# Kernel optimization log

Measured on AMD Instinct MI355X. Metric: run time of the kernel, lower is better.

Reference implementation:

```python
import jax, jax.numpy as jnp
import numpy as np

N_ENC = 500_000
N_PAT = 100_000
D_IN = 64
HID = 128
E = 1_000_000


def _seg_mean(x_src, src, dst, n_dst):
    # gather source features along edges, then segment-mean onto destinations
    msg = x_src[src]                                          # [E, d]
    s = jax.ops.segment_sum(msg, dst, num_segments=n_dst)     # [n_dst, d]
    cnt = jax.ops.segment_sum(jnp.ones((src.shape[0], 1), x_src.dtype), dst,
                              num_segments=n_dst)             # [n_dst, 1]
    return s / jnp.maximum(cnt, 1.0)


def _sage(x_src, x_dst, src, dst, n_dst, Wl, Wr, b):
    # PyG SAGEConv: lin_l(mean_aggr(x_j)) + lin_r(x_i); lin_l has bias, lin_r none
    agg = _seg_mean(x_src, src, dst, n_dst)
    return agg @ Wl + b + x_dst @ Wr


def setup_inputs() -> dict:
    key = jax.random.key(0)
    ks = jax.random.split(key, 24)
    sc = 0.05
    inp = {
        "x_enc": jax.random.normal(ks[0], (N_ENC, D_IN), jnp.float32),
        "x_pat": jax.random.normal(ks[1], (N_PAT, D_IN), jnp.float32),
        "src_pe": jax.random.randint(ks[2], (E,), 0, N_PAT),
        "dst_pe": jax.random.randint(ks[3], (E,), 0, N_ENC),
        "src_ep": jax.random.randint(ks[4], (E,), 0, N_ENC),
        "dst_ep": jax.random.randint(ks[5], (E,), 0, N_PAT),
        # layer 1, per edge type
        "Wl_pe1": jax.random.normal(ks[6], (D_IN, HID), jnp.float32) * sc,
        "Wr_pe1": jax.random.normal(ks[7], (D_IN, HID), jnp.float32) * sc,
        "b_pe1": jnp.zeros((HID,), jnp.float32),
        "Wl_ep1": jax.random.normal(ks[8], (D_IN, HID), jnp.float32) * sc,
        "Wr_ep1": jax.random.normal(ks[9], (D_IN, HID), jnp.float32) * sc,
        "b_ep1": jnp.zeros((HID,), jnp.float32),
        # layer 2, per edge type
        "Wl_pe2": jax.random.normal(ks[10], (HID, HID), jnp.float32) * sc,
        "Wr_pe2": jax.random.normal(ks[11], (HID, HID), jnp.float32) * sc,
        "b_pe2": jnp.zeros((HID,), jnp.float32),
        "Wl_ep2": jax.random.normal(ks[12], (HID, HID), jnp.float32) * sc,
        "Wr_ep2": jax.random.normal(ks[13], (HID, HID), jnp.float32) * sc,
        "b_ep2": jnp.zeros((HID,), jnp.float32),
        # classifier
        "Wc": jax.random.normal(ks[14], (HID, 1), jnp.float32) * sc,
        "bc": jnp.zeros((1,), jnp.float32),
    }
    return inp


def reference(x_enc, x_pat, src_pe, dst_pe, src_ep, dst_ep,
              Wl_pe1, Wr_pe1, b_pe1, Wl_ep1, Wr_ep1, b_ep1,
              Wl_pe2, Wr_pe2, b_pe2, Wl_ep2, Wr_ep2, b_ep2,
              Wc, bc):
    # layer 1 (hetero: one SAGEConv per edge type; each node type has one incoming relation)
    h_enc = jax.nn.relu(_sage(x_pat, x_enc, src_pe, dst_pe, N_ENC, Wl_pe1, Wr_pe1, b_pe1))
    h_pat = jax.nn.relu(_sage(x_enc, x_pat, src_ep, dst_ep, N_PAT, Wl_ep1, Wr_ep1, b_ep1))
    # layer 2
    h_enc2 = _sage(h_pat, h_enc, src_pe, dst_pe, N_ENC, Wl_pe2, Wr_pe2, b_pe2)
    # classifier on encounter nodes -> flat logits
    logit = (h_enc2 @ Wc + bc).reshape(-1)                    # [N_ENC]
    return logit
```

## Files before the change

### kernel.cpp

```cpp
#include <hip/hip_runtime.h>
#include <hip/hip_bf16.h>

#define N_ENC 500000
#define N_PAT 100000
#define N_TOT 600000
#define D 64
#define HID 128
#define NE 1000000

#define NB_ENC 245
#define NB 441
#define CAP 8192
#define CH 8192

typedef unsigned short ushort_t;
typedef unsigned int uint_t;
typedef __attribute__((ext_vector_type(8))) short bfrag8;
typedef __attribute__((ext_vector_type(4))) float f32x4;

#define OFF_CURSOR   0
#define ZERO_FLOATS  512
#define OFF_BBASE    512
#define OFF_BASE     1024
#define OFF_CSR      601056
#define OFF_XBF_ENC  2601056
#define OFF_BIN      2601056
#define OFF_XBF_PAT  18601056
#define OFF_SPAT     21801056
#define OFF_FRAGS    21901056
#define OFF_WL2C     21917440
#define OFF_WR2C     21917568
#define OFF_C0       21917696

__device__ inline ushort_t f2bf(float x) {
    uint_t u = __float_as_uint(x);
    u += 0x7fffu + ((u >> 16) & 1u);
    return (ushort_t)(u >> 16);
}

__global__ __launch_bounds__(256) void prep_kernel(
    const float* __restrict__ Wl_pe1, const float* __restrict__ Wr_pe1,
    const float* __restrict__ Wl_ep1, const float* __restrict__ Wr_ep1,
    const float* __restrict__ Wl_pe2, const float* __restrict__ Wr_pe2,
    const float* __restrict__ b_pe2, const float* __restrict__ Wc,
    const float* __restrict__ bc, float* __restrict__ ws)
{
    int t = blockIdx.x * blockDim.x + threadIdx.x;
    const int total = 4 * 8192;
    ushort_t* fr = (ushort_t*)(ws + OFF_FRAGS);
    for (int i = t; i < total; i += gridDim.x * blockDim.x) {
        int mtx = i >> 13;
        int r = i & 8191;
        int jj = r & 7;
        int l = (r >> 3) & 63;
        int ft = r >> 9;
        int kt = ft & 1;
        int jt = ft >> 1;
        int k = kt * 32 + (l >> 4) * 8 + jj;
        int j = jt * 16 + (l & 15);
        const float* W = (mtx == 0) ? Wl_pe1 : (mtx == 1) ? Wr_pe1
                       : (mtx == 2) ? Wl_ep1 : Wr_ep1;
        fr[i] = f2bf(W[k * HID + j]);
    }
    if (blockIdx.x == 0) {
        int tid = threadIdx.x;
        if (tid < HID) {
            float s1 = 0.f, s2 = 0.f;
            for (int j = 0; j < HID; j++) {
                float wc = Wc[j];
                s1 += Wl_pe2[tid * HID + j] * wc;
                s2 += Wr_pe2[tid * HID + j] * wc;
            }
            ws[OFF_WL2C + tid] = s1;
            ws[OFF_WR2C + tid] = s2;
            if (tid == 0) {
                float c0 = bc[0];
                for (int j = 0; j < HID; j++) c0 += b_pe2[j] * Wc[j];
                ws[OFF_C0] = c0;
            }
        }
    }
}

__global__ __launch_bounds__(256) void cvt_bf16_all_kernel(
    const float* __restrict__ x_enc, const float* __restrict__ x_pat,
    ushort_t* __restrict__ xbf_enc, ushort_t* __restrict__ xbf_pat)
{
    const int n8_enc = N_ENC * D / 8;
    const int n8_tot = n8_enc + N_PAT * D / 8;
    int stride = gridDim.x * 256;
    for (int i = blockIdx.x * 256 + threadIdx.x; i < n8_tot; i += stride) {
        const float* in; ushort_t* outp; int j;
        if (i < n8_enc) { in = x_enc; outp = xbf_enc; j = i; }
        else            { in = x_pat; outp = xbf_pat; j = i - n8_enc; }
        const f32x4* p = (const f32x4*)(in + (size_t)j * 8);
        f32x4 v0 = p[0], v1 = p[1];
        uint4 o;
        o.x = (uint_t)f2bf(v0[0]) | ((uint_t)f2bf(v0[1]) << 16);
        o.y = (uint_t)f2bf(v0[2]) | ((uint_t)f2bf(v0[3]) << 16);
        o.z = (uint_t)f2bf(v1[0]) | ((uint_t)f2bf(v1[1]) << 16);
        o.w = (uint_t)f2bf(v1[2]) | ((uint_t)f2bf(v1[3]) << 16);
        *(uint4*)(outp + (size_t)j * 8) = o;
    }
}


__global__ __launch_bounds__(256) void bin_kernel(
    const int* __restrict__ src_pe, const int* __restrict__ dst_pe,
    const int* __restrict__ src_ep, const int* __restrict__ dst_ep,
    int* __restrict__ cursor, uint_t* __restrict__ bin)
{
    __shared__ int lhist[512];
    __shared__ int lbase[512];
    __shared__ int lcnt2[NB];
    __shared__ int gpos[NB];
    __shared__ int s[256];
    __shared__ uint_t lout[CH];
    int t = threadIdx.x;
    int e0 = blockIdx.x * CH;
    int n = min(CH, 2 * NE - e0);

    for (int i = t; i < 512; i += 256) lhist[i] = 0;
    for (int i = t; i < NB; i += 256) lcnt2[i] = 0;
    __syncthreads();
    for (int i = t; i < n; i += 256) {
        int e = e0 + i;
        int dc = (e < NE) ? dst_pe[e] : N_ENC + dst_ep[e - NE];
        int b = (dc < N_ENC) ? (dc >> 11) : (NB_ENC + ((dc - N_ENC) >> 9));
        atomicAdd(&lhist[b], 1);
    }
    __syncthreads();
    int a0 = lhist[2 * t], a1 = lhist[2 * t + 1];
    s[t] = a0 + a1;
    __syncthreads();
    for (int off = 1; off < 256; off <<= 1) {
        int u = (t >= off) ? s[t - off] : 0;
        __syncthreads();
        s[t] += u;
        __syncthreads();
    }
    int ex = s[t] - a0 - a1;
    lbase[2 * t] = ex;
    lbase[2 * t + 1] = ex + a0;
    __syncthreads();
    for (int b = t; b < NB; b += 256) {
        int c = lhist[b];
        if (c) gpos[b] = atomicAdd(&cursor[b], c);
    }
    __syncthreads();
    for (int i = t; i < n; i += 256) {
        int e = e0 + i;
        int dc, sv;
        if (e < NE) { dc = dst_pe[e]; sv = src_pe[e]; }
        else { dc = N_ENC + dst_ep[e - NE]; sv = src_ep[e - NE]; }
        int b, loc;
        if (dc < N_ENC) { b = dc >> 11; loc = dc & 2047; }
        else { b = NB_ENC + ((dc - N_ENC) >> 9); loc = (dc - N_ENC) & 511; }
        int r = atomicAdd(&lcnt2[b], 1);
        lout[lbase[b] + r] = (uint_t)sv | ((uint_t)loc << 20);
    }
    __syncthreads();
    int wv = t >> 6, ln = t & 63;
    for (int b = wv; b < NB; b += 4) {
        int c = lhist[b];
        if (!c) continue;
        int gp = gpos[b];
        int c2 = min(c, CAP - gp);
        if (c2 <= 0) continue;
        uint_t* dstp = bin + (size_t)b * CAP + gp;
        const uint_t* srcp = lout + lbase[b];
        for (int k = ln; k < c2; k += 64) dstp[k] = srcp[k];
    }
}

__global__ __launch_bounds__(256) void bucketscan_kernel(
    const int* __restrict__ cursor, int* __restrict__ bbase,
    int* __restrict__ base)
{
    __shared__ int s[256];
    __shared__ int c2[512];
    int t = threadIdx.x;
    for (int i = t; i < 512; i += 256) c2[i] = (i < NB) ? min(cursor[i], CAP) : 0;
    __syncthreads();
    int a0 = c2[2 * t], a1 = c2[2 * t + 1];
    s[t] = a0 + a1;
    __syncthreads();
    for (int off = 1; off < 256; off <<= 1) {
        int u = (t >= off) ? s[t - off] : 0;
        __syncthreads();
        s[t] += u;
        __syncthreads();
    }
    int ex = s[t] - a0 - a1;
    if (2 * t < NB) bbase[2 * t] = ex;
    if (2 * t + 1 < NB) bbase[2 * t + 1] = ex + a0;
    if (t == 255) { bbase[NB] = s[t]; base[N_TOT] = s[t]; }
}

__global__ __launch_bounds__(256) void csrbuild_kernel(
    const uint_t* __restrict__ bin, const int* __restrict__ cursor,
    const int* __restrict__ bbase, int* __restrict__ base,
    int* __restrict__ csr)
{
    __shared__ int h[2048];
    __shared__ int nb_[2048];
    __shared__ int s[256];
    __shared__ uint_t lout[CAP];
    int b = blockIdx.x;
    int t = threadIdx.x;
    int cnt = min(cursor[b], CAP);
    int nodes_base, nnodes;
    if (b < NB_ENC) { nodes_base = b << 11; nnodes = min(2048, N_ENC - nodes_base); }
    else { nodes_base = N_ENC + ((b - NB_ENC) << 9); nnodes = min(512, N_TOT - nodes_base); }
    const uint_t* reg = bin + (size_t)b * CAP;

    for (int i = t; i < 2048; i += 256) h[i] = 0;
    __syncthreads();
    for (int i = t; i < cnt; i += 256) atomicAdd(&h[reg[i] >> 20], 1);
    __syncthreads();
    int loc[8];
    int sum = 0;
#pragma unroll
    for (int j = 0; j < 8; j++) { loc[j] = sum; sum += h[8 * t + j]; }
    s[t] = sum;
    __syncthreads();
    for (int off = 1; off < 256; off <<= 1) {
        int u = (t >= off) ? s[t - off] : 0;
        __syncthreads();
        s[t] += u;
        __syncthreads();
    }
    int ex = s[t] - sum;
#pragma unroll
    for (int j = 0; j < 8; j++) nb_[8 * t + j] = ex + loc[j];
    __syncthreads();
    int gb = bbase[b];
    for (int i = t; i < nnodes; i += 256) base[nodes_base + i] = gb + nb_[i];
    for (int i = t; i < 2048; i += 256) h[i] = 0;
    __syncthreads();
    for (int i = t; i < cnt; i += 256) {
        uint_t p = reg[i];
        int lc = p >> 20;
        int r = atomicAdd(&h[lc], 1);
        lout[nb_[lc] + r] = p & 0xFFFFFu;
    }
    __syncthreads();
    for (int k = t; k < cnt; k += 256) csr[gb + k] = (int)lout[k];
}

__global__ __launch_bounds__(256) void transform_fused_kernel(
    const ushort_t* __restrict__ xsrc, const int* __restrict__ csr,
    const int* __restrict__ base, const ushort_t* __restrict__ xdst,
    const ushort_t* __restrict__ fragWl, const ushort_t* __restrict__ fragWr,
    const float* __restrict__ bias, const float* __restrict__ cvec,
    const float* __restrict__ sval, const float* __restrict__ c0p,
    float* __restrict__ out, int nwaves, int add_extra)
{
    int wid = blockIdx.x * 4 + (threadIdx.x >> 6);
    if (wid >= nwaves) return;
    int l = threadIdx.x & 63;
    int m = l & 15;
    int q = l >> 4;
    int nb = wid * 16;
    int row = nb + m;

    int s0 = base[row], s1 = base[row + 1];
    float degf = (float)(s1 - s0);

    const ushort_t* xd = xdst + (size_t)row * D;
    bfrag8 x0 = *(const bfrag8*)(xd + q * 8);
    bfrag8 x1 = *(const bfrag8*)(xd + 32 + q * 8);

    float accf[16];
#pragma unroll
    for (int i = 0; i < 16; i++) accf[i] = 0.f;
    float sa = 0.f;

    int s1m1 = s1 - 1;
    for (int e = s0; e < s1; e += 4) {
        int sidx[4];
#pragma unroll
        for (int i = 0; i < 4; i++) {
            int ee = e + i;
            sidx[i] = csr[ee < s1m1 ? ee : s1m1];
        }
        uint4 w0[4], w1[4];
        float sv[4];
#pragma unroll
        for (int i = 0; i < 4; i++) {
            const uint_t* xr = (const uint_t*)(xsrc + (size_t)sidx[i] * D);
            w0[i] = *(const uint4*)(xr + q * 4);
            w1[i] = *(const uint4*)(xr + 16 + q * 4);
            sv[i] = (add_extra && q == 0) ? sval[sidx[i]] : 0.f;
        }
#pragma unroll
        for (int i = 0; i < 4; i++) {
            if (e + i < s1) {
                uint_t dw[8] = {w0[i].x, w0[i].y, w0[i].z, w0[i].w,
                                w1[i].x, w1[i].y, w1[i].z, w1[i].w};
#pragma unroll
                for (int k = 0; k < 8; k++) {
                    accf[2 * k]     += __uint_as_float(dw[k] << 16);
                    accf[2 * k + 1] += __uint_as_float(dw[k] & 0xffff0000u);
                }
                sa += sv[i];
            }
        }
    }

    bfrag8 a0, a1;
#pragma unroll
    for (int i = 0; i < 8; i++) {
        a0[i] = (short)f2bf(accf[i]);
        a1[i] = (short)f2bf(accf[8 + i]);
    }

    float bias_v[8], cvec_v[8];
#pragma unroll
    for (int jt = 0; jt < 8; jt++) {
        bias_v[jt] = bias[jt * 16 + m];
        cvec_v[jt] = cvec[jt * 16 + m];
    }

    f32x4 invc4;
#pragma unroll
    for (int r = 0; r < 4; r++) {
        float dg = __shfl(degf, q * 4 + r);
        invc4[r] = 1.0f / fmaxf(dg, 1.0f);
    }

    f32x4 p = {0.f, 0.f, 0.f, 0.f};
#pragma unroll
    for (int jt = 0; jt < 8; jt++) {
        const bfrag8* bl0 = (const bfrag8*)(fragWl + ((size_t)(jt * 2 + 0) * 64 + l) * 8);
        const bfrag8* bl1 = (const bfrag8*)(fragWl + ((size_t)(jt * 2 + 1) * 64 + l) * 8);
        const bfrag8* br0 = (const bfrag8*)(fragWr + ((size_t)(jt * 2 + 0) * 64 + l) * 8);
        const bfrag8* br1 = (const bfrag8*)(fragWr + ((size_t)(jt * 2 + 1) * 64 + l) * 8);
        f32x4 accl = {0.f, 0.f, 0.f, 0.f};
        f32x4 accr = {0.f, 0.f, 0.f, 0.f};
        accl = __builtin_amdgcn_mfma_f32_16x16x32_bf16(a0, *bl0, accl, 0, 0, 0);
        accl = __builtin_amdgcn_mfma_f32_16x16x32_bf16(a1, *bl1, accl, 0, 0, 0);
        accr = __builtin_amdgcn_mfma_f32_16x16x32_bf16(x0, *br0, accr, 0, 0, 0);
        accr = __builtin_amdgcn_mfma_f32_16x16x32_bf16(x1, *br1, accr, 0, 0, 0);
        float bj = bias_v[jt], cj = cvec_v[jt];
#pragma unroll
        for (int r = 0; r < 4; r++) {
            float z = accl[r] * invc4[r] + accr[r] + bj;
            p[r] += fmaxf(z, 0.f) * cj;
        }
    }
#pragma unroll
    for (int off = 1; off < 16; off <<= 1) {
        p[0] += __shfl_xor(p[0], off, 16);
        p[1] += __shfl_xor(p[1], off, 16);
        p[2] += __shfl_xor(p[2], off, 16);
        p[3] += __shfl_xor(p[3], off, 16);
    }
    f32x4 sa4;
#pragma unroll
    for (int r = 0; r < 4; r++) sa4[r] = __shfl(sa, q * 4 + r);
    if (m == 0) {
        int basen = nb + q * 4;
        f32x4 o = p;
        if (add_extra) {
            float c0 = c0p[0];
#pragma unroll
            for (int r = 0; r < 4; r++)
                o[r] += sa4[r] * invc4[r] + c0;
        }
        *(f32x4*)(out + basen) = o;
    }
}

extern "C" void kernel_launch(void* const* d_in, const int* in_sizes, int n_in,
                              void* d_out, int out_size, void* d_ws, size_t ws_size,
                              hipStream_t stream)
{
    const float* x_enc  = (const float*)d_in[0];
    const float* x_pat  = (const float*)d_in[1];
    const int*   src_pe = (const int*)d_in[2];
    const int*   dst_pe = (const int*)d_in[3];
    const int*   src_ep = (const int*)d_in[4];
    const int*   dst_ep = (const int*)d_in[5];
    const float* Wl_pe1 = (const float*)d_in[6];
    const float* Wr_pe1 = (const float*)d_in[7];
    const float* b_pe1  = (const float*)d_in[8];
    const float* Wl_ep1 = (const float*)d_in[9];
    const float* Wr_ep1 = (const float*)d_in[10];
    const float* b_ep1  = (const float*)d_in[11];
    const float* Wl_pe2 = (const float*)d_in[12];
    const float* Wr_pe2 = (const float*)d_in[13];
    const float* b_pe2  = (const float*)d_in[14];
    const float* Wc = (const float*)d_in[18];
    const float* bc = (const float*)d_in[19];

    float* ws  = (float*)d_ws;
    float* out = (float*)d_out;

    hipMemsetAsync(d_ws, 0, (size_t)ZERO_FLOATS * sizeof(float), stream);

    prep_kernel<<<128, 256, 0, stream>>>(Wl_pe1, Wr_pe1, Wl_ep1, Wr_ep1,
                                         Wl_pe2, Wr_pe2, b_pe2, Wc, bc, ws);

    int* cursor = (int*)(ws + OFF_CURSOR);
    int* bbase  = (int*)(ws + OFF_BBASE);
    int* basep  = (int*)(ws + OFF_BASE);
    int* csr    = (int*)(ws + OFF_CSR);
    uint_t* bin = (uint_t*)(ws + OFF_BIN);
    ushort_t* xbf_enc = (ushort_t*)(ws + OFF_XBF_ENC);
    ushort_t* xbf_pat = (ushort_t*)(ws + OFF_XBF_PAT);

    int nchunks = (2 * NE + CH - 1) / CH;
    bin_kernel<<<nchunks, 256, 0, stream>>>(src_pe, dst_pe, src_ep, dst_ep,
                                            cursor, bin);

    bucketscan_kernel<<<1, 256, 0, stream>>>(cursor, bbase, basep);

    csrbuild_kernel<<<NB, 256, 0, stream>>>(bin, cursor, bbase, basep, csr);

    cvt_bf16_all_kernel<<<2048, 256, 0, stream>>>(x_enc, x_pat, xbf_enc, xbf_pat);

    const ushort_t* frags = (const ushort_t*)(ws + OFF_FRAGS);

    int pat_waves = N_PAT / 16;
    transform_fused_kernel<<<(pat_waves + 3) / 4, 256, 0, stream>>>(
        xbf_enc, csr, basep + N_ENC, xbf_pat,
        frags + 2 * 8192, frags + 3 * 8192, b_ep1, ws + OFF_WL2C,
        nullptr, nullptr, ws + OFF_SPAT, pat_waves, 0);

    int enc_waves = N_ENC / 16;
    transform_fused_kernel<<<(enc_waves + 3) / 4, 256, 0, stream>>>(
        xbf_pat, csr, basep, xbf_enc,
        frags + 0 * 8192, frags + 1 * 8192, b_pe1, ws + OFF_WR2C,
        ws + OFF_SPAT, ws + OFF_C0, out, enc_waves, 1);
}
```

Before: 478.4 us.

## Fold weight prep into bin kernel and bucket scan into CSR build

Weight fragment conversion and classifier folding now run in extra blocks appended to the binning kernel instead of a separate prep launch. Every CSR-build block now recomputes the 441-entry bucket prefix scan itself, which removes the single-block bucketscan kernel. Together this cuts two launches and their serialization gaps. The transform kernel also hoists the bias and cvec loads and has all lanes load sval, at the cost of redundant scan work per block and extra loads.

```diff
diff --git a/kernel.cpp b/kernel.cpp
--- a/kernel.cpp
+++ b/kernel.cpp
@@ -12,6 +12,8 @@
 #define NB 441
 #define CAP 8192
 #define CH 8192
+#define NCHUNKS 245
+#define PREP_BLOCKS 33
 
 typedef unsigned short ushort_t;
 typedef unsigned int uint_t;
@@ -20,7 +22,6 @@
 
 #define OFF_CURSOR   0
 #define ZERO_FLOATS  512
-#define OFF_BBASE    512
 #define OFF_BASE     1024
 #define OFF_CSR      601056
 #define OFF_XBF_ENC  2601056
@@ -36,50 +37,6 @@
     uint_t u = __float_as_uint(x);
     u += 0x7fffu + ((u >> 16) & 1u);
     return (ushort_t)(u >> 16);
-}
-
-__global__ __launch_bounds__(256) void prep_kernel(
-    const float* __restrict__ Wl_pe1, const float* __restrict__ Wr_pe1,
-    const float* __restrict__ Wl_ep1, const float* __restrict__ Wr_ep1,
-    const float* __restrict__ Wl_pe2, const float* __restrict__ Wr_pe2,
-    const float* __restrict__ b_pe2, const float* __restrict__ Wc,
-    const float* __restrict__ bc, float* __restrict__ ws)
-{
-    int t = blockIdx.x * blockDim.x + threadIdx.x;
-    const int total = 4 * 8192;
-    ushort_t* fr = (ushort_t*)(ws + OFF_FRAGS);
-    for (int i = t; i < total; i += gridDim.x * blockDim.x) {
-        int mtx = i >> 13;
-        int r = i & 8191;
-        int jj = r & 7;
-        int l = (r >> 3) & 63;
-        int ft = r >> 9;
-        int kt = ft & 1;
-        int jt = ft >> 1;
-        int k = kt * 32 + (l >> 4) * 8 + jj;
-        int j = jt * 16 + (l & 15);
-        const float* W = (mtx == 0) ? Wl_pe1 : (mtx == 1) ? Wr_pe1
-                       : (mtx == 2) ? Wl_ep1 : Wr_ep1;
-        fr[i] = f2bf(W[k * HID + j]);
-    }
-    if (blockIdx.x == 0) {
-        int tid = threadIdx.x;
-        if (tid < HID) {
-            float s1 = 0.f, s2 = 0.f;
-            for (int j = 0; j < HID; j++) {
-                float wc = Wc[j];
-                s1 += Wl_pe2[tid * HID + j] * wc;
-                s2 += Wr_pe2[tid * HID + j] * wc;
-            }
-            ws[OFF_WL2C + tid] = s1;
-            ws[OFF_WR2C + tid] = s2;
-            if (tid == 0) {
-                float c0 = bc[0];
-                for (int j = 0; j < HID; j++) c0 += b_pe2[j] * Wc[j];
-                ws[OFF_C0] = c0;
-            }
-        }
-    }
 }
 
 __global__ __launch_bounds__(256) void cvt_bf16_all_kernel(
@@ -104,11 +61,15 @@
     }
 }
 
-
-__global__ __launch_bounds__(256) void bin_kernel(
+__global__ __launch_bounds__(256) void bin_prep_kernel(
     const int* __restrict__ src_pe, const int* __restrict__ dst_pe,
     const int* __restrict__ src_ep, const int* __restrict__ dst_ep,
-    int* __restrict__ cursor, uint_t* __restrict__ bin)
+    int* __restrict__ cursor, uint_t* __restrict__ bin,
+    const float* __restrict__ Wl_pe1, const float* __restrict__ Wr_pe1,
+    const float* __restrict__ Wl_ep1, const float* __restrict__ Wr_ep1,
+    const float* __restrict__ Wl_pe2, const float* __restrict__ Wr_pe2,
+    const float* __restrict__ b_pe2, const float* __restrict__ Wc,
+    const float* __restrict__ bc, float* __restrict__ ws)
 {
     __shared__ int lhist[512];
     __shared__ int lbase[512];
@@ -117,6 +78,46 @@
     __shared__ int s[256];
     __shared__ uint_t lout[CH];
     int t = threadIdx.x;
+
+    if (blockIdx.x >= NCHUNKS) {
+        int pb = blockIdx.x - NCHUNKS;
+        ushort_t* fr = (ushort_t*)(ws + OFF_FRAGS);
+        if (pb < 32) {
+            const int total = 4 * 8192;
+            for (int i = pb * 256 + t; i < total; i += 32 * 256) {
+                int mtx = i >> 13;
+                int r = i & 8191;
+                int jj = r & 7;
+                int l = (r >> 3) & 63;
+                int ft = r >> 9;
+                int kt = ft & 1;
+                int jt = ft >> 1;
+                int k = kt * 32 + (l >> 4) * 8 + jj;
+                int j = jt * 16 + (l & 15);
+                const float* W = (mtx == 0) ? Wl_pe1 : (mtx == 1) ? Wr_pe1
+                               : (mtx == 2) ? Wl_ep1 : Wr_ep1;
+                fr[i] = f2bf(W[k * HID + j]);
+            }
+        } else {
+            if (t < HID) {
+                float s1 = 0.f, s2 = 0.f;
+                for (int j = 0; j < HID; j++) {
+                    float wc = Wc[j];
+                    s1 += Wl_pe2[t * HID + j] * wc;
+                    s2 += Wr_pe2[t * HID + j] * wc;
+                }
+                ws[OFF_WL2C + t] = s1;
+                ws[OFF_WR2C + t] = s2;
+                if (t == 0) {
+                    float c0 = bc[0];
+                    for (int j = 0; j < HID; j++) c0 += b_pe2[j] * Wc[j];
+                    ws[OFF_C0] = c0;
+                }
+            }
+        }
+        return;
+    }
+
     int e0 = blockIdx.x * CH;
     int n = min(CH, 2 * NE - e0);
 
@@ -173,41 +174,38 @@
     }
 }
 
-__global__ __launch_bounds__(256) void bucketscan_kernel(
-    const int* __restrict__ cursor, int* __restrict__ bbase,
-    int* __restrict__ base)
-{
-    __shared__ int s[256];
-    __shared__ int c2[512];
-    int t = threadIdx.x;
-    for (int i = t; i < 512; i += 256) c2[i] = (i < NB) ? min(cursor[i], CAP) : 0;
-    __syncthreads();
-    int a0 = c2[2 * t], a1 = c2[2 * t + 1];
-    s[t] = a0 + a1;
-    __syncthreads();
-    for (int off = 1; off < 256; off <<= 1) {
-        int u = (t >= off) ? s[t - off] : 0;
-        __syncthreads();
-        s[t] += u;
-        __syncthreads();
-    }
-    int ex = s[t] - a0 - a1;
-    if (2 * t < NB) bbase[2 * t] = ex;
-    if (2 * t + 1 < NB) bbase[2 * t + 1] = ex + a0;
-    if (t == 255) { bbase[NB] = s[t]; base[N_TOT] = s[t]; }
-}
-
 __global__ __launch_bounds__(256) void csrbuild_kernel(
     const uint_t* __restrict__ bin, const int* __restrict__ cursor,
-    const int* __restrict__ bbase, int* __restrict__ base,
-    int* __restrict__ csr)
+    int* __restrict__ base, int* __restrict__ csr)
 {
     __shared__ int h[2048];
     __shared__ int nb_[2048];
     __shared__ int s[256];
+    __shared__ int cs[512];
     __shared__ uint_t lout[CAP];
     int b = blockIdx.x;
     int t = threadIdx.x;
+
+    for (int i = t; i < 512; i += 256) cs[i] = (i < NB) ? min(cursor[i], CAP) : 0;
+    __syncthreads();
+    int ca0 = cs[2 * t], ca1 = cs[2 * t + 1];
+    s[t] = ca0 + ca1;
+    __syncthreads();
+    for (int off = 1; off < 256; off <<= 1) {
+        int u = (t >= off) ? s[t - off] : 0;
+        __syncthreads();
+        s[t] += u;
+        __syncthreads();
+    }
+    int cex = s[t] - ca0 - ca1;
+    int ctotal = s[255];
+    __syncthreads();
+    cs[2 * t] = cex;
+    cs[2 * t + 1] = cex + ca0;
+    __syncthreads();
+    int gb = cs[b];
+    if (b == 0 && t == 0) base[N_TOT] = ctotal;
+
     int cnt = min(cursor[b], CAP);
     int nodes_base, nnodes;
     if (b < NB_ENC) { nodes_base = b << 11; nnodes = min(2048, N_ENC - nodes_base); }
@@ -234,7 +232,6 @@
 #pragma unroll
     for (int j = 0; j < 8; j++) nb_[8 * t + j] = ex + loc[j];
     __syncthreads();
-    int gb = bbase[b];
     for (int i = t; i < nnodes; i += 256) base[nodes_base + i] = gb + nb_[i];
     for (int i = t; i < 2048; i += 256) h[i] = 0;
     __syncthreads();
@@ -271,6 +268,13 @@
     bfrag8 x0 = *(const bfrag8*)(xd + q * 8);
     bfrag8 x1 = *(const bfrag8*)(xd + 32 + q * 8);
 
+    float bias_v[8], cvec_v[8];
+#pragma unroll
+    for (int jt = 0; jt < 8; jt++) {
+        bias_v[jt] = bias[jt * 16 + m];
+        cvec_v[jt] = cvec[jt * 16 + m];
+    }
+
     float accf[16];
 #pragma unroll
     for (int i = 0; i < 16; i++) accf[i] = 0.f;
@@ -291,7 +295,7 @@
             const uint_t* xr = (const uint_t*)(xsrc + (size_t)sidx[i] * D);
             w0[i] = *(const uint4*)(xr + q * 4);
             w1[i] = *(const uint4*)(xr + 16 + q * 4);
-            sv[i] = (add_extra && q == 0) ? sval[sidx[i]] : 0.f;
+            if (add_extra) sv[i] = sval[sidx[i]];
         }
 #pragma unroll
         for (int i = 0; i < 4; i++) {
@@ -303,7 +307,7 @@
                     accf[2 * k]     += __uint_as_float(dw[k] << 16);
                     accf[2 * k + 1] += __uint_as_float(dw[k] & 0xffff0000u);
                 }
-                sa += sv[i];
+                if (add_extra) sa += sv[i];
             }
         }
     }
@@ -313,13 +317,6 @@
     for (int i = 0; i < 8; i++) {
         a0[i] = (short)f2bf(accf[i]);
         a1[i] = (short)f2bf(accf[8 + i]);
-    }
-
-    float bias_v[8], cvec_v[8];
-#pragma unroll
-    for (int jt = 0; jt < 8; jt++) {
-        bias_v[jt] = bias[jt * 16 + m];
-        cvec_v[jt] = cvec[jt * 16 + m];
     }
 
     f32x4 invc4;
@@ -399,24 +396,18 @@
 
     hipMemsetAsync(d_ws, 0, (size_t)ZERO_FLOATS * sizeof(float), stream);
 
-    prep_kernel<<<128, 256, 0, stream>>>(Wl_pe1, Wr_pe1, Wl_ep1, Wr_ep1,
-                                         Wl_pe2, Wr_pe2, b_pe2, Wc, bc, ws);
-
     int* cursor = (int*)(ws + OFF_CURSOR);
-    int* bbase  = (int*)(ws + OFF_BBASE);
     int* basep  = (int*)(ws + OFF_BASE);
     int* csr    = (int*)(ws + OFF_CSR);
     uint_t* bin = (uint_t*)(ws + OFF_BIN);
     ushort_t* xbf_enc = (ushort_t*)(ws + OFF_XBF_ENC);
     ushort_t* xbf_pat = (ushort_t*)(ws + OFF_XBF_PAT);
 
-    int nchunks = (2 * NE + CH - 1) / CH;
-    bin_kernel<<<nchunks, 256, 0, stream>>>(src_pe, dst_pe, src_ep, dst_ep,
-                                            cursor, bin);
-
-    bucketscan_kernel<<<1, 256, 0, stream>>>(cursor, bbase, basep);
-
-    csrbuild_kernel<<<NB, 256, 0, stream>>>(bin, cursor, bbase, basep, csr);
+    bin_prep_kernel<<<NCHUNKS + PREP_BLOCKS, 256, 0, stream>>>(
+        src_pe, dst_pe, src_ep, dst_ep, cursor, bin,
+        Wl_pe1, Wr_pe1, Wl_ep1, Wr_ep1, Wl_pe2, Wr_pe2, b_pe2, Wc, bc, ws);
+
+    csrbuild_kernel<<<NB, 256, 0, stream>>>(bin, cursor, basep, csr);
 
     cvt_bf16_all_kernel<<<2048, 256, 0, stream>>>(x_enc, x_pat, xbf_enc, xbf_pat);
 
```

Result: faster. 449.5 us (-6.0%).
